# Optimization experiments

Measured on AMD Instinct MI355X. Metric: run time of the kernel, lower is better.

The kernel has to match this reference:

```python
import jax, jax.numpy as jnp
import numpy as np

SMOOTH_STEP_PARAM = 1.0  # = 1/gamma in the TEL paper
DEPTH = 6


def smooth_step(x):
    # TEL smooth-step: 0 for u<=-1/2, 1 for u>=1/2, cubic -2u^3+1.5u+0.5 inside.
    u = SMOOTH_STEP_PARAM * x
    inner = (-2.0 * u + 1.5) * u * u + (u + 0.5) * 0.0 + (-2.0 * u ** 3 + 1.5 * u + 0.5)
    # use single clean expression for the cubic
    cubic = -2.0 * u ** 3 + 1.5 * u + 0.5
    return jnp.where(u <= -0.5, 0.0, jnp.where(u >= 0.5, 1.0, cubic))


def setup_inputs() -> dict:
    key = jax.random.key(0)
    k1, k2, k3 = jax.random.split(key, 3)
    B, D, T, O = 32768, 1024, 8, 128
    num_leaves = 2 ** DEPTH
    x = jax.random.normal(k1, (B, D), dtype=jnp.float32)
    # RandomUniform(-0.01, 0.01) initializers in the original layer
    node_weights = jax.random.uniform(k2, (T, D, num_leaves - 1), dtype=jnp.float32,
                                      minval=-0.01, maxval=0.01)
    leaf_weights = jax.random.uniform(k3, (T, O, num_leaves), dtype=jnp.float32,
                                      minval=-0.01, maxval=0.01)
    return {"x": x, "node_weights": node_weights, "leaf_weights": leaf_weights}


def reference(x, node_weights, leaf_weights):
    B = x.shape[0]
    T = node_weights.shape[0]
    # routing probabilities at every internal node (BFS order): [B, T, 2^depth-1]
    s = smooth_step(jnp.einsum('bd,tdi->bti', x, node_weights))
    # accumulate leaf reach probabilities level by level (left child gets s)
    mu = jnp.ones((B, T, 1), dtype=x.dtype)
    start = 0
    for level in range(DEPTH):
        width = 2 ** level
        s_lvl = s[:, :, start:start + width]           # [B, T, width]
        mu = jnp.stack([mu * s_lvl, mu * (1.0 - s_lvl)], axis=-1)
        mu = mu.reshape(B, T, 2 * width)
        start += width
    # weighted sum of leaf vectors, summed over trees (sum_outputs=True)
    return jnp.einsum('btl,tol->bo', mu, leaf_weights)
```

## Files before the change

kernel.cpp:

```cpp
#include <hip/hip_runtime.h>
#include <hip/hip_bf16.h>
#include <stdint.h>

#define KDIM 1024
#define TSTR 72
#define RSTR 576

typedef __attribute__((ext_vector_type(4))) float f32x4;
typedef __attribute__((ext_vector_type(8))) short bf16x8;

#define WS_LB_OFF ((size_t)1 << 20)

__device__ __forceinline__ unsigned short f2bf_rne(float f) {
    unsigned u = __float_as_uint(f);
    u = (u + 0x7fffu + ((u >> 16) & 1u)) >> 16;
    return (unsigned short)u;
}

__device__ __forceinline__ unsigned int pack2_bf16(float a, float b) {
    __hip_bfloat162 h = __float22bfloat162_rn(make_float2(a, b));
    union { __hip_bfloat162 h; unsigned int u; } cv;
    cv.h = h;
    return cv.u;
}

__device__ __forceinline__ float gs_get(const uint4* q, int i) {
    uint4 v = q[i >> 3];
    int c = (i >> 1) & 3;
    unsigned w = (c == 0) ? v.x : (c == 1) ? v.y : (c == 2) ? v.z : v.w;
    return __uint_as_float((i & 1) ? (w & 0xffff0000u) : (w << 16));
}

__device__ __forceinline__ bf16x8 cvt8(f32x4 lo, f32x4 hi) {
    union { uint4 u; bf16x8 v; } cv;
    cv.u.x = pack2_bf16(lo[0], lo[1]);
    cv.u.y = pack2_bf16(lo[2], lo[3]);
    cv.u.z = pack2_bf16(hi[0], hi[1]);
    cv.u.w = pack2_bf16(hi[2], hi[3]);
    return cv.v;
}

__global__ void prep_w(const float* __restrict__ nw, unsigned short* __restrict__ wb) {
    int idx = blockIdx.x * 256 + threadIdx.x;
    int e    = idx & 7;
    int lane = (idx >> 3) & 63;
    int cb   = (idx >> 9) & 31;
    int ks   = idx >> 14;
    int col = cb * 16 + (lane & 15);
    int k   = ks * 32 + (lane >> 4) * 8 + e;
    int t = col >> 6, i = col & 63;
    float v = (i < 63) ? nw[(t * KDIM + k) * 63 + i] : 0.0f;
    wb[idx] = f2bf_rne(v);
}

__global__ void prep_l(const float* __restrict__ lw, unsigned short* __restrict__ lb) {
    int idx = blockIdx.x * 256 + threadIdx.x;
    int e    = idx & 7;
    int lane = (idx >> 3) & 63;
    int obk  = (idx >> 9) & 7;
    int kq   = idx >> 12;
    int o = obk * 16 + (lane & 15);
    int c = kq * 32 + (lane >> 4) * 8 + e;
    int t = c >> 6, l = c & 63;
    lb[idx] = f2bf_rne(lw[(t * 128 + o) * 64 + l]);
}

__launch_bounds__(256, 2)
__global__ void fused(const float* __restrict__ x, const unsigned short* __restrict__ wb,
                      const unsigned short* __restrict__ lb, float* __restrict__ out) {
    __shared__ __align__(16) unsigned short st[32 * RSTR];

    const int tid  = threadIdx.x;
    const int wave = tid >> 6, lane = tid & 63;
    const int quad = lane >> 4, l16 = lane & 15;
    const int mb   = blockIdx.x;

    f32x4 acc[8][4];
    const f32x4 z4 = {0.f, 0.f, 0.f, 0.f};
    #pragma unroll
    for (int a = 0; a < 8; ++a)
        #pragma unroll
        for (int b = 0; b < 4; ++b) acc[a][b] = z4;

    const float* xr0 = x + (size_t)(mb * 64 + 0 * 16 + l16) * KDIM + quad * 8;
    const float* xr1 = x + (size_t)(mb * 64 + 1 * 16 + l16) * KDIM + quad * 8;
    const float* xr2 = x + (size_t)(mb * 64 + 2 * 16 + l16) * KDIM + quad * 8;
    const float* xr3 = x + (size_t)(mb * 64 + 3 * 16 + l16) * KDIM + quad * 8;
    const unsigned short* wb0 = wb + (size_t)(wave * 8 * 64 + lane) * 8;

    for (int ks = 0; ks < 32; ++ks) {
        bf16x8 af[8], bf[4];
        {
            f32x4 lo, hi;
            lo = *(const f32x4*)(xr0 + ks * 32); hi = *(const f32x4*)(xr0 + ks * 32 + 4);
            bf[0] = cvt8(lo, hi);
            lo = *(const f32x4*)(xr1 + ks * 32); hi = *(const f32x4*)(xr1 + ks * 32 + 4);
            bf[1] = cvt8(lo, hi);
            lo = *(const f32x4*)(xr2 + ks * 32); hi = *(const f32x4*)(xr2 + ks * 32 + 4);
            bf[2] = cvt8(lo, hi);
            lo = *(const f32x4*)(xr3 + ks * 32); hi = *(const f32x4*)(xr3 + ks * 32 + 4);
            bf[3] = cvt8(lo, hi);
        }
        const unsigned short* wbase = wb0 + (size_t)ks * 16384;
        #pragma unroll
        for (int ct = 0; ct < 8; ++ct)
            af[ct] = *(const bf16x8*)(wbase + ct * 512);
        #pragma unroll
        for (int ct = 0; ct < 8; ++ct)
            #pragma unroll
            for (int rt = 0; rt < 4; ++rt)
                acc[ct][rt] = __builtin_amdgcn_mfma_f32_16x16x32_bf16(af[ct], bf[rt], acc[ct][rt], 0, 0, 0);
    }

    #pragma unroll
    for (int p = 0; p < 2; ++p) {
        __syncthreads();
        #pragma unroll
        for (int rt2 = 0; rt2 < 2; ++rt2) {
            int rowl = rt2 * 16 + l16;
            #pragma unroll
            for (int ct = 0; ct < 8; ++ct) {
                int colb = wave * 128 + ct * 16 + quad * 4;
                f32x4 a = acc[ct][p * 2 + rt2];
                float s0[4];
                #pragma unroll
                for (int j = 0; j < 4; ++j) {
                    float u = a[j];
                    u = fminf(fmaxf(u, -0.5f), 0.5f);
                    s0[j] = u * (1.5f - 2.0f * u * u) + 0.5f;
                }
                uint2 pk;
                pk.x = pack2_bf16(s0[0], s0[1]);
                pk.y = pack2_bf16(s0[2], s0[3]);
                *(uint2*)&st[rowl * RSTR + (colb >> 6) * TSTR + (colb & 63)] = pk;
            }
        }
        __syncthreads();
        {
            int r = tid >> 3, t = tid & 7;
            unsigned short* base = &st[r * RSTR + t * TSTR];
            uint4 q[8];
            #pragma unroll
            for (int c = 0; c < 8; ++c) q[c] = *(const uint4*)(base + c * 8);
            float mu[32];
            mu[0] = 1.0f;
            int start = 0;
            #pragma unroll
            for (int lvl = 0; lvl < 5; ++lvl) {
                int width = 1 << lvl;
                #pragma unroll
                for (int j = width - 1; j >= 0; --j) {
                    float m = mu[j], s_ = gs_get(q, start + j);
                    mu[2 * j + 1] = m * (1.0f - s_);
                    mu[2 * j]     = m * s_;
                }
                start += width;
            }
            #pragma unroll
            for (int c = 0; c < 8; ++c) {
                unsigned pk2[4];
                #pragma unroll
                for (int e = 0; e < 4; ++e) {
                    int j = c * 4 + e;
                    float m = mu[j], s_ = gs_get(q, 31 + j);
                    pk2[e] = pack2_bf16(m * s_, m * (1.0f - s_));
                }
                uint4 v; v.x = pk2[0]; v.y = pk2[1]; v.z = pk2[2]; v.w = pk2[3];
                *(uint4*)(base + c * 8) = v;
            }
        }
        __syncthreads();
        {
            int rtile = wave & 1, obw = wave >> 1;
            f32x4 a2[4];
            a2[0] = z4; a2[1] = z4; a2[2] = z4; a2[3] = z4;
            #pragma unroll
            for (int kq = 0; kq < 16; ++kq) {
                int c0 = kq * 32 + quad * 8;
                bf16x8 bmu = *(const bf16x8*)&st[(rtile * 16 + l16) * RSTR + (c0 >> 6) * TSTR + (c0 & 63)];
                const unsigned short* lbase = lb + ((size_t)((kq * 8 + obw * 4) * 64 + lane)) * 8;
                #pragma unroll
                for (int ct = 0; ct < 4; ++ct) {
                    bf16x8 alf = *(const bf16x8*)(lbase + ct * 512);
                    a2[ct] = __builtin_amdgcn_mfma_f32_16x16x32_bf16(alf, bmu, a2[ct], 0, 0, 0);
                }
            }
            #pragma unroll
            for (int ct = 0; ct < 4; ++ct) {
                int rowg = mb * 64 + p * 32 + rtile * 16 + l16;
                int og = obw * 64 + ct * 16 + quad * 4;
                *(f32x4*)(out + (size_t)rowg * 128 + og) = a2[ct];
            }
        }
    }
}

extern "C" void kernel_launch(void* const* d_in, const int* in_sizes, int n_in,
                              void* d_out, int out_size, void* d_ws, size_t ws_size,
                              hipStream_t stream) {
    const float* x  = (const float*)d_in[0];
    const float* nw = (const float*)d_in[1];
    const float* lw = (const float*)d_in[2];
    float* out = (float*)d_out;

    unsigned short* wb = (unsigned short*)d_ws;
    unsigned short* lb = (unsigned short*)((char*)d_ws + WS_LB_OFF);

    prep_w<<<2048, 256, 0, stream>>>(nw, wb);
    prep_l<<<256, 256, 0, stream>>>(lw, lb);
    fused<<<512, 256, 0, stream>>>(x, wb, lb, out);
}
```

Baseline: 274.1 us.

## Stage x tile in LDS as bf16 and spread GEMM over 16 waves

The fused kernel now launches 1024 threads per block instead of 256. It converts the 64-row x tile to bf16 once into shared memory in two K halves, where before every wave reloaded and converted x from global memory. Each wave now owns 2 column tiles instead of 8, which cuts accumulator registers and is meant to raise occupancy and latency hiding. The costs are extra LDS (about 66KB for the x tile), more barriers, and a mu computation that runs on only a quarter of the threads.

```diff
diff --git a/kernel.cpp b/kernel.cpp
--- a/kernel.cpp
+++ b/kernel.cpp
@@ -3,6 +3,7 @@
 #include <stdint.h>
 
 #define KDIM 1024
+#define XSTR2 520
 #define TSTR 72
 #define RSTR 576
 
@@ -29,15 +30,6 @@
     int c = (i >> 1) & 3;
     unsigned w = (c == 0) ? v.x : (c == 1) ? v.y : (c == 2) ? v.z : v.w;
     return __uint_as_float((i & 1) ? (w & 0xffff0000u) : (w << 16));
-}
-
-__device__ __forceinline__ bf16x8 cvt8(f32x4 lo, f32x4 hi) {
-    union { uint4 u; bf16x8 v; } cv;
-    cv.u.x = pack2_bf16(lo[0], lo[1]);
-    cv.u.y = pack2_bf16(lo[2], lo[3]);
-    cv.u.z = pack2_bf16(hi[0], hi[1]);
-    cv.u.w = pack2_bf16(hi[2], hi[3]);
-    return cv.v;
 }
 
 __global__ void prep_w(const float* __restrict__ nw, unsigned short* __restrict__ wb) {
@@ -65,9 +57,10 @@
     lb[idx] = f2bf_rne(lw[(t * 128 + o) * 64 + l]);
 }
 
-__launch_bounds__(256, 2)
+__launch_bounds__(1024, 4)
 __global__ void fused(const float* __restrict__ x, const unsigned short* __restrict__ wb,
                       const unsigned short* __restrict__ lb, float* __restrict__ out) {
+    __shared__ __align__(16) unsigned short xs[64 * XSTR2];
     __shared__ __align__(16) unsigned short st[32 * RSTR];
 
     const int tid  = threadIdx.x;
@@ -75,52 +68,56 @@
     const int quad = lane >> 4, l16 = lane & 15;
     const int mb   = blockIdx.x;
 
-    f32x4 acc[8][4];
+    f32x4 acc[2][4];
     const f32x4 z4 = {0.f, 0.f, 0.f, 0.f};
     #pragma unroll
-    for (int a = 0; a < 8; ++a)
+    for (int a = 0; a < 2; ++a)
         #pragma unroll
         for (int b = 0; b < 4; ++b) acc[a][b] = z4;
 
-    const float* xr0 = x + (size_t)(mb * 64 + 0 * 16 + l16) * KDIM + quad * 8;
-    const float* xr1 = x + (size_t)(mb * 64 + 1 * 16 + l16) * KDIM + quad * 8;
-    const float* xr2 = x + (size_t)(mb * 64 + 2 * 16 + l16) * KDIM + quad * 8;
-    const float* xr3 = x + (size_t)(mb * 64 + 3 * 16 + l16) * KDIM + quad * 8;
-    const unsigned short* wb0 = wb + (size_t)(wave * 8 * 64 + lane) * 8;
-
-    for (int ks = 0; ks < 32; ++ks) {
-        bf16x8 af[8], bf[4];
-        {
-            f32x4 lo, hi;
-            lo = *(const f32x4*)(xr0 + ks * 32); hi = *(const f32x4*)(xr0 + ks * 32 + 4);
-            bf[0] = cvt8(lo, hi);
-            lo = *(const f32x4*)(xr1 + ks * 32); hi = *(const f32x4*)(xr1 + ks * 32 + 4);
-            bf[1] = cvt8(lo, hi);
-            lo = *(const f32x4*)(xr2 + ks * 32); hi = *(const f32x4*)(xr2 + ks * 32 + 4);
-            bf[2] = cvt8(lo, hi);
-            lo = *(const f32x4*)(xr3 + ks * 32); hi = *(const f32x4*)(xr3 + ks * 32 + 4);
-            bf[3] = cvt8(lo, hi);
-        }
-        const unsigned short* wbase = wb0 + (size_t)ks * 16384;
+    const int srow = tid >> 4, sf4 = tid & 15;
+    const float* xgr = x + (size_t)(mb * 64 + srow) * KDIM;
+    const unsigned short* wb0 = wb + ((size_t)(wave * 2) * 64 + lane) * 8;
+
+    for (int h = 0; h < 2; ++h) {
+        if (h) __syncthreads();
         #pragma unroll
-        for (int ct = 0; ct < 8; ++ct)
-            af[ct] = *(const bf16x8*)(wbase + ct * 512);
-        #pragma unroll
-        for (int ct = 0; ct < 8; ++ct)
+        for (int seg = 0; seg < 8; ++seg) {
+            int f4 = sf4 + seg * 16;
+            float4 v = *(const float4*)(xgr + h * 512 + f4 * 4);
+            uint2 pk;
+            pk.x = pack2_bf16(v.x, v.y);
+            pk.y = pack2_bf16(v.z, v.w);
+            *(uint2*)&xs[srow * XSTR2 + f4 * 4] = pk;
+        }
+        __syncthreads();
+        #pragma unroll 4
+        for (int ksl = 0; ksl < 16; ++ksl) {
+            const int ks = h * 16 + ksl;
+            bf16x8 bf[4], af[2];
             #pragma unroll
             for (int rt = 0; rt < 4; ++rt)
-                acc[ct][rt] = __builtin_amdgcn_mfma_f32_16x16x32_bf16(af[ct], bf[rt], acc[ct][rt], 0, 0, 0);
+                bf[rt] = *(const bf16x8*)&xs[(rt * 16 + l16) * XSTR2 + ksl * 32 + quad * 8];
+            const unsigned short* wbase = wb0 + (size_t)ks * 16384;
+            af[0] = *(const bf16x8*)(wbase);
+            af[1] = *(const bf16x8*)(wbase + 512);
+            #pragma unroll
+            for (int ct = 0; ct < 2; ++ct)
+                #pragma unroll
+                for (int rt = 0; rt < 4; ++rt)
+                    acc[ct][rt] = __builtin_amdgcn_mfma_f32_16x16x32_bf16(af[ct], bf[rt], acc[ct][rt], 0, 0, 0);
+        }
     }
 
     #pragma unroll
     for (int p = 0; p < 2; ++p) {
-        __syncthreads();
+        if (p) __syncthreads();
         #pragma unroll
         for (int rt2 = 0; rt2 < 2; ++rt2) {
-            int rowl = rt2 * 16 + l16;
-            #pragma unroll
-            for (int ct = 0; ct < 8; ++ct) {
-                int colb = wave * 128 + ct * 16 + quad * 4;
+            int r = rt2 * 16 + l16;
+            #pragma unroll
+            for (int ct = 0; ct < 2; ++ct) {
+                int colb = wave * 32 + ct * 16 + quad * 4;
                 f32x4 a = acc[ct][p * 2 + rt2];
                 float s0[4];
                 #pragma unroll
@@ -132,11 +129,11 @@
                 uint2 pk;
                 pk.x = pack2_bf16(s0[0], s0[1]);
                 pk.y = pack2_bf16(s0[2], s0[3]);
-                *(uint2*)&st[rowl * RSTR + (colb >> 6) * TSTR + (colb & 63)] = pk;
+                *(uint2*)&st[r * RSTR + (colb >> 6) * TSTR + (colb & 63)] = pk;
             }
         }
         __syncthreads();
-        {
+        if (tid < 256) {
             int r = tid >> 3, t = tid & 7;
             unsigned short* base = &st[r * RSTR + t * TSTR];
             uint4 q[8];
@@ -171,26 +168,19 @@
         }
         __syncthreads();
         {
-            int rtile = wave & 1, obw = wave >> 1;
-            f32x4 a2[4];
-            a2[0] = z4; a2[1] = z4; a2[2] = z4; a2[3] = z4;
+            int rtile = wave & 1, obk = wave >> 1;
+            int mr = rtile * 16 + l16;
+            f32x4 a2 = z4;
             #pragma unroll
             for (int kq = 0; kq < 16; ++kq) {
                 int c0 = kq * 32 + quad * 8;
-                bf16x8 bmu = *(const bf16x8*)&st[(rtile * 16 + l16) * RSTR + (c0 >> 6) * TSTR + (c0 & 63)];
-                const unsigned short* lbase = lb + ((size_t)((kq * 8 + obw * 4) * 64 + lane)) * 8;
-                #pragma unroll
-                for (int ct = 0; ct < 4; ++ct) {
-                    bf16x8 alf = *(const bf16x8*)(lbase + ct * 512);
-                    a2[ct] = __builtin_amdgcn_mfma_f32_16x16x32_bf16(alf, bmu, a2[ct], 0, 0, 0);
-                }
-            }
-            #pragma unroll
-            for (int ct = 0; ct < 4; ++ct) {
-                int rowg = mb * 64 + p * 32 + rtile * 16 + l16;
-                int og = obw * 64 + ct * 16 + quad * 4;
-                *(f32x4*)(out + (size_t)rowg * 128 + og) = a2[ct];
-            }
+                bf16x8 bmu = *(const bf16x8*)&st[mr * RSTR + (c0 >> 6) * TSTR + (c0 & 63)];
+                bf16x8 alf = *(const bf16x8*)(lb + ((size_t)((kq * 8 + obk) * 64 + lane)) * 8);
+                a2 = __builtin_amdgcn_mfma_f32_16x16x32_bf16(alf, bmu, a2, 0, 0, 0);
+            }
+            int rowg = mb * 64 + p * 32 + rtile * 16 + l16;
+            int og = obk * 16 + quad * 4;
+            *(f32x4*)(out + (size_t)rowg * 128 + og) = a2;
         }
     }
 }
@@ -208,5 +198,5 @@
 
     prep_w<<<2048, 256, 0, stream>>>(nw, wb);
     prep_l<<<256, 256, 0, stream>>>(lw, lb);
-    fused<<<512, 256, 0, stream>>>(x, wb, lb, out);
-}
+    fused<<<512, 1024, 0, stream>>>(x, wb, lb, out);
+}
```

Measured after the change: 250.4 us. 1.09x faster.
